# Kernel optimization log

Hardware: AMD Instinct MI355X
Metric: run time of the kernel (lower is better)

The kernel has to match this reference:

```python
import jax, jax.numpy as jnp
import numpy as np

N, E, D, L = 50000, 800000, 128, 2
EPS = 1e-7

def _logmap0(y):
    # Poincare ball (c=1) logmap at origin: artanh(||y||) * y / ||y||
    n = jnp.linalg.norm(y, axis=-1, keepdims=True)
    nc = jnp.clip(n, EPS, 1.0 - 1e-5)
    return jnp.arctanh(nc) * y / jnp.maximum(n, EPS)

def _expmap0(u):
    # Poincare ball (c=1) expmap at origin: tanh(||u||) * u / ||u||
    n = jnp.linalg.norm(u, axis=-1, keepdims=True)
    return jnp.tanh(n) * u / jnp.maximum(n, EPS)

def _l2norm(x):
    # F.normalize(p=2, dim=1)
    return x / jnp.maximum(jnp.linalg.norm(x, axis=1, keepdims=True), 1e-12)

def setup_inputs() -> dict:
    key = jax.random.key(0)
    ks = jax.random.split(key, 12)
    src = jax.random.randint(ks[0], (E,), 0, N)
    dst = jax.random.randint(ks[1], (E,), 0, N)
    e_emb = jax.random.normal(ks[2], (N, D), jnp.float32)
    b_emb = jax.random.normal(ks[3], (N, D), jnp.float32) * 0.1  # inside Poincare ball
    s_emb = jax.random.normal(ks[4], (N, D), jnp.float32)
    sc = 0.05
    eW = jax.random.normal(ks[5], (L, D, D), jnp.float32) * sc
    eB = jax.random.normal(ks[6], (L, D), jnp.float32) * sc
    bW = jax.random.normal(ks[7], (L, D, D), jnp.float32) * sc
    bB = jax.random.normal(ks[8], (L, D), jnp.float32) * sc
    sW = jax.random.normal(ks[9], (L, D, D), jnp.float32) * sc
    sB = jax.random.normal(ks[10], (L, D), jnp.float32) * sc
    return dict(e_emb=e_emb, b_emb=b_emb, s_emb=s_emb, eW=eW, eB=eB,
                bW=bW, bB=bB, sW=sW, sB=sB, src=src, dst=dst)

def reference(e_emb, b_emb, s_emb, eW, eB, bW, bB, sW, sB, src, dst):
    n_nodes = e_emb.shape[0]
    ones_e = jnp.ones(src.shape[0], jnp.float32)
    in_deg = jax.ops.segment_sum(ones_e, dst, num_segments=n_nodes)
    out_deg = jax.ops.segment_sum(ones_e, src, num_segments=n_nodes)
    # DGL GraphConv norm='both': D_out^{-1/2} (sum over in-neighbors) D_in^{-1/2}
    norm_out = jnp.where(out_deg > 0, out_deg ** -0.5, 0.0)[:, None]
    norm_in = jnp.where(in_deg > 0, in_deg ** -0.5, 0.0)[:, None]
    inv_in = jnp.where(in_deg > 0, 1.0 / in_deg, 0.0)[:, None]  # mean reduce

    def agg_sum(h):
        return jax.ops.segment_sum(h[src], dst, num_segments=n_nodes)

    for l in range(L):
        # Euclidean branch: GraphConv(norm='both') then LeakyReLU(0.2)
        h = agg_sum(e_emb * norm_out) * norm_in
        e_emb = jax.nn.leaky_relu(h @ eW[l].T + eB[l], negative_slope=0.2)
        # Hyperbolic branch: logmap0 -> Linear -> neighbor mean -> expmap0
        tan_b = _logmap0(b_emb) @ bW[l].T + bB[l]
        b_emb = _expmap0(agg_sum(tan_b) * inv_in)
        # Spherical branch: normalize -> Linear -> neighbor mean -> normalize
        tan_s = _l2norm(s_emb) @ sW[l].T + sB[l]
        s_emb = _l2norm(agg_sum(tan_s) * inv_in)
    return (e_emb, b_emb, s_emb)
```

## Files before the change

### kernel.cpp

```cpp
#include <hip/hip_runtime.h>
#include <math.h>

#define DD 128
#define PSTRIDE 384

typedef _Float16 half8 __attribute__((ext_vector_type(8)));
typedef float floatx4 __attribute__((ext_vector_type(4)));

__device__ __forceinline__ float g16_sum(float x) {
#pragma unroll
  for (int m = 8; m >= 1; m >>= 1) x += __shfl_xor(x, m, 64);
  return x;
}
__device__ __forceinline__ int wave_sum_i(int x) {
#pragma unroll
  for (int m = 32; m >= 1; m >>= 1) x += __shfl_xor(x, m, 64);
  return x;
}

__global__ void deg_wcvt_kernel(const int* __restrict__ src, const int* __restrict__ dst,
                                int* __restrict__ out_deg8, int* __restrict__ in_deg8,
                                int* __restrict__ rank8, int E, int N,
                                const float* __restrict__ eW, const float* __restrict__ bW,
                                const float* __restrict__ sW, _Float16* __restrict__ Wh, int nW,
                                int DB) {
  int bx = blockIdx.x;
  if (bx < DB) {
    int e = bx * 256 + threadIdx.x;
    if (e < E) {
      int h = e & 7;
      atomicAdd(&out_deg8[h * N + src[e]], 1);
      rank8[e] = atomicAdd(&in_deg8[h * N + dst[e]], 1);
    }
  } else {
    int i = (bx - DB) * 256 + threadIdx.x;
    if (i < nW) {
      Wh[i]          = (_Float16)eW[i];
      Wh[i + nW]     = (_Float16)bW[i];
      Wh[i + 2 * nW] = (_Float16)sW[i];
    }
  }
}

__global__ void norms_psum_kernel(const int* __restrict__ in_deg8, const int* __restrict__ out_deg8,
                                  int* __restrict__ in_deg, float* __restrict__ norm_in,
                                  float* __restrict__ norm_out, float* __restrict__ inv_in,
                                  int* __restrict__ part, int N) {
  __shared__ int wsum[4];
  int t = threadIdx.x, lane = t & 63, w = t >> 6;
  int i = blockIdx.x * 256 + t;
  int di = 0;
  if (i < N) {
    int dq = 0;
#pragma unroll
    for (int h = 0; h < 8; ++h) {
      di += in_deg8[h * N + i];
      dq += out_deg8[h * N + i];
    }
    in_deg[i] = di;
    norm_in[i]  = di > 0 ? 1.0f / sqrtf((float)di) : 0.0f;
    norm_out[i] = dq > 0 ? 1.0f / sqrtf((float)dq) : 0.0f;
    inv_in[i]   = di > 0 ? 1.0f / (float)di : 0.0f;
  }
  int s = wave_sum_i(di);
  if (lane == 0) wsum[w] = s;
  __syncthreads();
  if (t == 0) part[blockIdx.x] = wsum[0] + wsum[1] + wsum[2] + wsum[3];
}

__global__ void part_scan_kernel(int* __restrict__ part, int nb) {
  __shared__ int wsum[4];
  int t = threadIdx.x, lane = t & 63, w = t >> 6;
  int x = (t < nb) ? part[t] : 0;
  int v = x;
#pragma unroll
  for (int off = 1; off < 64; off <<= 1) {
    int y = __shfl_up(v, off, 64);
    if (lane >= off) v += y;
  }
  if (lane == 63) wsum[w] = v;
  __syncthreads();
  int base = 0;
  for (int j = 0; j < w; ++j) base += wsum[j];
  if (t < nb) part[t] = base + v - x;
}

__global__ void local_scan_kernel(const int* __restrict__ deg, const int* __restrict__ part,
                                  int* __restrict__ row_off, int* __restrict__ in_deg8,
                                  int N, int E) {
  __shared__ int wsum[4];
  int t = threadIdx.x, lane = t & 63, w = t >> 6;
  int i = blockIdx.x * 256 + t;
  int x = (i < N) ? deg[i] : 0;
  int v = x;
#pragma unroll
  for (int off = 1; off < 64; off <<= 1) {
    int y = __shfl_up(v, off, 64);
    if (lane >= off) v += y;
  }
  if (lane == 63) wsum[w] = v;
  __syncthreads();
  int base = 0;
  for (int j = 0; j < w; ++j) base += wsum[j];
  if (i < N) {
    int ro = part[blockIdx.x] + base + v - x;
    row_off[i] = ro;
    int cum = ro;
#pragma unroll
    for (int h = 0; h < 8; ++h) {
      int c = in_deg8[h * N + i];
      in_deg8[h * N + i] = cum;
      cum += c;
    }
  }
  if (blockIdx.x == 0 && t == 0) row_off[N] = E;
}

__device__ __forceinline__ void gemm0_tile(int part, int rb, const float* __restrict__ A,
                                           const _Float16* __restrict__ Wh,
                                           const float* __restrict__ Bb,
                                           _Float16* __restrict__ Q, int N) {
  int t = threadIdx.x, lane = t & 63, w = t >> 6;
  int m = lane & 15, quad = lane >> 4, c0 = w * 32;
  int rbase = rb * 64;
  _Float16* Qo = Q + part * DD;
  half8 bf[2][4];
#pragma unroll
  for (int tj = 0; tj < 2; ++tj)
#pragma unroll
    for (int kk = 0; kk < 4; ++kk)
      bf[tj][kk] = *(const half8*)&Wh[(c0 + tj * 16 + m) * DD + kk * 32 + quad * 8];
  float bias0 = 0.f, bias1 = 0.f;
  if (part) { bias0 = Bb[c0 + m]; bias1 = Bb[c0 + 16 + m]; }
#pragma unroll
  for (int r = 0; r < 4; ++r) {
    int row0 = r * 16;
    int arow = rbase + row0 + m; if (arow >= N) arow = N - 1;
    const float* Ap = A + (size_t)arow * DD;
    half8 af[4];
    float nsq = 0.f;
#pragma unroll
    for (int kk = 0; kk < 4; ++kk) {
      float4 x0 = *(const float4*)&Ap[kk * 32 + quad * 8];
      float4 x1 = *(const float4*)&Ap[kk * 32 + quad * 8 + 4];
      if (part)
        nsq += x0.x * x0.x + x0.y * x0.y + x0.z * x0.z + x0.w * x0.w +
               x1.x * x1.x + x1.y * x1.y + x1.z * x1.z + x1.w * x1.w;
      half8 a;
      a[0] = (_Float16)x0.x; a[1] = (_Float16)x0.y; a[2] = (_Float16)x0.z; a[3] = (_Float16)x0.w;
      a[4] = (_Float16)x1.x; a[5] = (_Float16)x1.y; a[6] = (_Float16)x1.z; a[7] = (_Float16)x1.w;
      af[kk] = a;
    }
    float fr = 1.f;
    if (part) {
      nsq += __shfl_xor(nsq, 16, 64);
      nsq += __shfl_xor(nsq, 32, 64);
      float n = sqrtf(nsq);
      if (part == 1) {
        float nc = fminf(fmaxf(n, 1e-7f), 1.0f - 1e-5f);
        fr = atanhf(nc) / fmaxf(n, 1e-7f);
      } else {
        fr = 1.0f / fmaxf(n, 1e-12f);
      }
    }
    floatx4 acc0 = {0.f, 0.f, 0.f, 0.f}, acc1 = {0.f, 0.f, 0.f, 0.f};
#pragma unroll
    for (int kk = 0; kk < 4; ++kk) {
      acc0 = __builtin_amdgcn_mfma_f32_16x16x32_f16(af[kk], bf[0][kk], acc0, 0, 0, 0);
      acc1 = __builtin_amdgcn_mfma_f32_16x16x32_f16(af[kk], bf[1][kk], acc1, 0, 0, 0);
    }
    int vrow = rbase + row0 + quad * 4;
#pragma unroll
    for (int reg = 0; reg < 4; ++reg) {
      int v = vrow + reg;
      float fs = part ? __shfl(fr, quad * 4 + reg, 64) : 1.f;
      if (v < N) {
        Qo[(size_t)v * PSTRIDE + c0 + m]      = (_Float16)(acc0[reg] * fs + bias0);
        Qo[(size_t)v * PSTRIDE + c0 + 16 + m] = (_Float16)(acc1[reg] * fs + bias1);
      }
    }
  }
}

__device__ __forceinline__ void gemm_tile(int part, int rb, const _Float16* __restrict__ P,
                                          const _Float16* __restrict__ Wh,
                                          const float* __restrict__ Bb,
                                          _Float16* __restrict__ Q, int N) {
  int t = threadIdx.x, lane = t & 63, w = t >> 6;
  int m = lane & 15, quad = lane >> 4, c0 = w * 32;
  int rbase = rb * 64;
  const _Float16* Ain = P + part * DD;
  _Float16* Qo = Q + part * DD;
  half8 bf[2][4];
#pragma unroll
  for (int tj = 0; tj < 2; ++tj)
#pragma unroll
    for (int kk = 0; kk < 4; ++kk)
      bf[tj][kk] = *(const half8*)&Wh[(c0 + tj * 16 + m) * DD + kk * 32 + quad * 8];
  float bias0 = 0.f, bias1 = 0.f;
  if (Bb) { bias0 = Bb[c0 + m]; bias1 = Bb[c0 + 16 + m]; }
#pragma unroll
  for (int r = 0; r < 4; ++r) {
    int row0 = r * 16;
    int arow = rbase + row0 + m; if (arow >= N) arow = N - 1;
    const _Float16* Ap = Ain + (size_t)arow * PSTRIDE;
    floatx4 acc0 = {0.f, 0.f, 0.f, 0.f}, acc1 = {0.f, 0.f, 0.f, 0.f};
#pragma unroll
    for (int kk = 0; kk < 4; ++kk) {
      half8 af = *(const half8*)&Ap[kk * 32 + quad * 8];
      acc0 = __builtin_amdgcn_mfma_f32_16x16x32_f16(af, bf[0][kk], acc0, 0, 0, 0);
      acc1 = __builtin_amdgcn_mfma_f32_16x16x32_f16(af, bf[1][kk], acc1, 0, 0, 0);
    }
    int vrow = rbase + row0 + quad * 4;
#pragma unroll
    for (int reg = 0; reg < 4; ++reg) {
      int v = vrow + reg;
      if (v < N) {
        Qo[(size_t)v * PSTRIDE + c0 + m]      = (_Float16)(acc0[reg] + bias0);
        Qo[(size_t)v * PSTRIDE + c0 + 16 + m] = (_Float16)(acc1[reg] + bias1);
      }
    }
  }
}

__global__ __launch_bounds__(256) void fill_gemm0_kernel(
    const int* __restrict__ src, const int* __restrict__ dst,
    const int* __restrict__ rank8, const int* __restrict__ bin_base,
    const float* __restrict__ norm_out, int2* __restrict__ csr_sw, int E,
    const float* __restrict__ e0, const float* __restrict__ b0, const float* __restrict__ s0,
    const _Float16* __restrict__ WhE, const _Float16* __restrict__ WhB,
    const _Float16* __restrict__ WhS, const float* __restrict__ bBl,
    const float* __restrict__ sBl, _Float16* __restrict__ Q, int N, int FB, int GB) {
  int bx = blockIdx.x;
  if (bx < FB) {
    int e = bx * 256 + threadIdx.x;
    if (e < E) {
      int d = dst[e], s = src[e];
      int h = e & 7;
      int pos = bin_base[h * N + d] + rank8[e];
      csr_sw[pos] = make_int2(s, __float_as_int(norm_out[s]));
    }
  } else {
    int gb = bx - FB;
    int part = gb / GB, rb = gb % GB;
    const float* A = (part == 0) ? e0 : (part == 1 ? b0 : s0);
    const _Float16* Wh = (part == 0) ? WhE : (part == 1 ? WhB : WhS);
    const float* Bb = (part == 0) ? nullptr : (part == 1 ? bBl : sBl);
    gemm0_tile(part, rb, A, Wh, Bb, Q, N);
  }
}

__global__ __launch_bounds__(256) void gemm3_kernel(const _Float16* __restrict__ P,
                                                    const _Float16* __restrict__ WhE,
                                                    const _Float16* __restrict__ WhB,
                                                    const _Float16* __restrict__ WhS,
                                                    const float* __restrict__ bBl,
                                                    const float* __restrict__ sBl,
                                                    _Float16* __restrict__ Q, int N) {
  int part = blockIdx.y;
  const _Float16* Wh = (part == 0) ? WhE : (part == 1 ? WhB : WhS);
  const float* Bb = (part == 0) ? nullptr : (part == 1 ? bBl : sBl);
  gemm_tile(part, blockIdx.x, P, Wh, Bb, Q, N);
}

__global__ __launch_bounds__(256) void agg_fused_kernel(
    const _Float16* __restrict__ Q, const int* __restrict__ row_off,
    const int2* __restrict__ csr_sw, const float* __restrict__ norm_in,
    const float* __restrict__ inv_in, const float* __restrict__ eBias,
    float* __restrict__ oe, float* __restrict__ ob, float* __restrict__ os,
    _Float16* __restrict__ Pnext, int N, int write_pack, int write_out) {
  int lane = threadIdx.x & 63;
  int v = blockIdx.x * 4 + (threadIdx.x >> 6);
  if (v >= N) return;
  int g = lane >> 4, q = lane & 15;
  int beg = row_off[v], end = row_off[v + 1];
  float eacc[8], bacc[8], sacc[8];
#pragma unroll
  for (int j = 0; j < 8; ++j) { eacc[j] = 0.f; bacc[j] = 0.f; sacc[j] = 0.f; }
  int i = beg;
  for (; i + 8 <= end; i += 8) {
    int2 swa = csr_sw[i + g];
    int2 swb = csr_sw[i + 4 + g];
    float wa = __int_as_float(swa.y), wb = __int_as_float(swb.y);
    const _Float16* ra = Q + (size_t)swa.x * PSTRIDE + q * 8;
    const _Float16* rb = Q + (size_t)swb.x * PSTRIDE + q * 8;
    half8 ea = *(const half8*)ra;
    half8 e2 = *(const half8*)rb;
    half8 ba = *(const half8*)(ra + 128);
    half8 b2 = *(const half8*)(rb + 128);
    half8 sa = *(const half8*)(ra + 256);
    half8 s2 = *(const half8*)(rb + 256);
#pragma unroll
    for (int j = 0; j < 8; ++j) {
      eacc[j] += wa * (float)ea[j];
      eacc[j] += wb * (float)e2[j];
      bacc[j] += (float)ba[j];
      bacc[j] += (float)b2[j];
      sacc[j] += (float)sa[j];
      sacc[j] += (float)s2[j];
    }
  }
  if (i + 4 <= end) {
    int2 sw = csr_sw[i + g];
    float wgt = __int_as_float(sw.y);
    const _Float16* rp = Q + (size_t)sw.x * PSTRIDE + q * 8;
    half8 ev = *(const half8*)rp;
    half8 bv = *(const half8*)(rp + 128);
    half8 sv = *(const half8*)(rp + 256);
#pragma unroll
    for (int j = 0; j < 8; ++j) {
      eacc[j] += wgt * (float)ev[j];
      bacc[j] += (float)bv[j];
      sacc[j] += (float)sv[j];
    }
    i += 4;
  }
  if (i + g < end) {
    int2 sw = csr_sw[i + g];
    float wgt = __int_as_float(sw.y);
    const _Float16* rp = Q + (size_t)sw.x * PSTRIDE + q * 8;
    half8 ev = *(const half8*)rp;
    half8 bv = *(const half8*)(rp + 128);
    half8 sv = *(const half8*)(rp + 256);
#pragma unroll
    for (int j = 0; j < 8; ++j) {
      eacc[j] += wgt * (float)ev[j];
      bacc[j] += (float)bv[j];
      sacc[j] += (float)sv[j];
    }
  }
#pragma unroll
  for (int j = 0; j < 8; ++j) {
    eacc[j] += __shfl_xor(eacc[j], 16, 64);
    eacc[j] += __shfl_xor(eacc[j], 32, 64);
    bacc[j] += __shfl_xor(bacc[j], 16, 64);
    bacc[j] += __shfl_xor(bacc[j], 32, 64);
    sacc[j] += __shfl_xor(sacc[j], 16, 64);
    sacc[j] += __shfl_xor(sacc[j], 32, 64);
  }
  float ni = norm_in[v], iv = inv_in[v];
  const float4* ebp = (const float4*)eBias;
  float4 eb0 = ebp[q * 2], eb1 = ebp[q * 2 + 1];
  float bias[8] = {eb0.x, eb0.y, eb0.z, eb0.w, eb1.x, eb1.y, eb1.z, eb1.w};
  float h[8], ub[8], us[8];
  float ss2 = 0.f;
#pragma unroll
  for (int j = 0; j < 8; ++j) {
    float t = eacc[j] * ni + bias[j];
    h[j] = t > 0.f ? t : 0.2f * t;
    ub[j] = bacc[j] * iv;
    us[j] = sacc[j] * iv; ss2 += us[j] * us[j];
  }
  float ns = sqrtf(g16_sum(ss2));
  float fs = 1.0f / fmaxf(ns, 1e-12f);
  if (write_out) {
    float bs2 = 0.f;
#pragma unroll
    for (int j = 0; j < 8; ++j) bs2 += ub[j] * ub[j];
    float nb = sqrtf(g16_sum(bs2));
    float fb = tanhf(nb) / fmaxf(nb, 1e-7f);
    if (g == 0) {
      float4* p = (float4*)(oe + (size_t)v * DD);
      p[q * 2]     = make_float4(h[0], h[1], h[2], h[3]);
      p[q * 2 + 1] = make_float4(h[4], h[5], h[6], h[7]);
    } else if (g == 1) {
      float4* p = (float4*)(ob + (size_t)v * DD);
      p[q * 2]     = make_float4(ub[0] * fb, ub[1] * fb, ub[2] * fb, ub[3] * fb);
      p[q * 2 + 1] = make_float4(ub[4] * fb, ub[5] * fb, ub[6] * fb, ub[7] * fb);
    } else if (g == 2) {
      float4* p = (float4*)(os + (size_t)v * DD);
      p[q * 2]     = make_float4(us[0] * fs, us[1] * fs, us[2] * fs, us[3] * fs);
      p[q * 2 + 1] = make_float4(us[4] * fs, us[5] * fs, us[6] * fs, us[7] * fs);
    }
  }
  if (write_pack) {
    if (g == 3) {
      half8 he, hb, hs;
#pragma unroll
      for (int j = 0; j < 8; ++j) {
        he[j] = (_Float16)h[j];
        hb[j] = (_Float16)ub[j];
        hs[j] = (_Float16)(us[j] * fs);
      }
      _Float16* Pr = Pnext + (size_t)v * PSTRIDE + q * 8;
      *(half8*)&Pr[0]   = he;
      *(half8*)&Pr[128] = hb;
      *(half8*)&Pr[256] = hs;
    }
  }
}

extern "C" void kernel_launch(void* const* d_in, const int* in_sizes, int n_in,
                              void* d_out, int out_size, void* d_ws, size_t ws_size,
                              hipStream_t stream) {
  const float* e0 = (const float*)d_in[0];
  const float* b0 = (const float*)d_in[1];
  const float* s0 = (const float*)d_in[2];
  const float* eW = (const float*)d_in[3];
  const float* eB = (const float*)d_in[4];
  const float* bW = (const float*)d_in[5];
  const float* bB = (const float*)d_in[6];
  const float* sW = (const float*)d_in[7];
  const float* sB = (const float*)d_in[8];
  const int* src = (const int*)d_in[9];
  const int* dst = (const int*)d_in[10];
  int N = in_sizes[0] / DD;
  int E = in_sizes[9];
  int L = in_sizes[3] / (DD * DD);
  int LDD2 = L * DD * DD;

  char* w = (char*)d_ws;
  int* in_deg8  = (int*)w; w += (size_t)8 * N * 4;
  int* out_deg8 = (int*)w; w += (size_t)8 * N * 4;
  int* rank8    = (int*)w; w += (size_t)E * 4;
  int* in_deg   = (int*)w; w += (size_t)N * 4;
  int* row_off  = (int*)w; w += (size_t)(N + 4) * 4;
  int* pscan    = (int*)w; w += (size_t)1024 * 4;
  int2* csr_sw  = (int2*)w; w += (size_t)E * 8;
  float* norm_in  = (float*)w; w += (size_t)N * 4;
  float* norm_out = (float*)w; w += (size_t)N * 4;
  float* inv_in   = (float*)w; w += (size_t)N * 4;
  w = (char*)(((size_t)w + 255) & ~(size_t)255);
  _Float16* P = (_Float16*)w; w += (size_t)N * PSTRIDE * 2;
  _Float16* Q = (_Float16*)w; w += (size_t)N * PSTRIDE * 2;
  _Float16* Wh = (_Float16*)w; w += (size_t)3 * LDD2 * 2;
  _Float16* whE = Wh;
  _Float16* whB = Wh + LDD2;
  _Float16* whS = Wh + 2 * LDD2;

  float* oe = (float*)d_out;
  float* ob = oe + (size_t)N * DD;
  float* os = ob + (size_t)N * DD;

  int DB = (E + 255) / 256;
  int AB = (N + 3) / 4;
  int GB = (N + 63) / 64;
  int WB = (LDD2 + 255) / 256;
  int PB = (N + 255) / 256;

  hipMemsetAsync(d_ws, 0, (size_t)16 * N * 4, stream);
  deg_wcvt_kernel<<<DB + WB, 256, 0, stream>>>(src, dst, out_deg8, in_deg8, rank8, E, N,
                                               eW, bW, sW, Wh, LDD2, DB);
  norms_psum_kernel<<<PB, 256, 0, stream>>>(in_deg8, out_deg8, in_deg,
                                            norm_in, norm_out, inv_in, pscan, N);
  part_scan_kernel<<<1, 256, 0, stream>>>(pscan, PB);
  local_scan_kernel<<<PB, 256, 0, stream>>>(in_deg, pscan, row_off, in_deg8, N, E);
  fill_gemm0_kernel<<<DB + 3 * GB, 256, 0, stream>>>(src, dst, rank8, in_deg8, norm_out,
                                                     csr_sw, E, e0, b0, s0,
                                                     whE, whB, whS, bB, sB, Q, N, DB, GB);
  agg_fused_kernel<<<AB, 256, 0, stream>>>(Q, row_off, csr_sw, norm_in, inv_in, eB,
                                           oe, ob, os, P, N,
                                           (L > 1) ? 1 : 0, (L == 1) ? 1 : 0);
  for (int l = 1; l < L; ++l) {
    size_t lo = (size_t)l * DD * DD;
    gemm3_kernel<<<dim3(GB, 3), 256, 0, stream>>>(P, whE + lo, whB + lo, whS + lo,
                                                  bB + (size_t)l * DD, sB + (size_t)l * DD, Q, N);
    agg_fused_kernel<<<AB, 256, 0, stream>>>(Q, row_off, csr_sw, norm_in, inv_in,
                                             eB + (size_t)l * DD, oe, ob, os, P, N,
                                             (l < L - 1) ? 1 : 0, (l == L - 1) ? 1 : 0);
  }
}
```

Before: 482.2 us.

## Fold source norm into GEMM output, shrink CSR to indices, overlap hyperbolic/spherical GEMM with degree pass

```diff
diff --git a/kernel.cpp b/kernel.cpp
--- a/kernel.cpp
+++ b/kernel.cpp
@@ -18,107 +18,9 @@
   return x;
 }
 
-__global__ void deg_wcvt_kernel(const int* __restrict__ src, const int* __restrict__ dst,
-                                int* __restrict__ out_deg8, int* __restrict__ in_deg8,
-                                int* __restrict__ rank8, int E, int N,
-                                const float* __restrict__ eW, const float* __restrict__ bW,
-                                const float* __restrict__ sW, _Float16* __restrict__ Wh, int nW,
-                                int DB) {
-  int bx = blockIdx.x;
-  if (bx < DB) {
-    int e = bx * 256 + threadIdx.x;
-    if (e < E) {
-      int h = e & 7;
-      atomicAdd(&out_deg8[h * N + src[e]], 1);
-      rank8[e] = atomicAdd(&in_deg8[h * N + dst[e]], 1);
-    }
-  } else {
-    int i = (bx - DB) * 256 + threadIdx.x;
-    if (i < nW) {
-      Wh[i]          = (_Float16)eW[i];
-      Wh[i + nW]     = (_Float16)bW[i];
-      Wh[i + 2 * nW] = (_Float16)sW[i];
-    }
-  }
-}
-
-__global__ void norms_psum_kernel(const int* __restrict__ in_deg8, const int* __restrict__ out_deg8,
-                                  int* __restrict__ in_deg, float* __restrict__ norm_in,
-                                  float* __restrict__ norm_out, float* __restrict__ inv_in,
-                                  int* __restrict__ part, int N) {
-  __shared__ int wsum[4];
-  int t = threadIdx.x, lane = t & 63, w = t >> 6;
-  int i = blockIdx.x * 256 + t;
-  int di = 0;
-  if (i < N) {
-    int dq = 0;
-#pragma unroll
-    for (int h = 0; h < 8; ++h) {
-      di += in_deg8[h * N + i];
-      dq += out_deg8[h * N + i];
-    }
-    in_deg[i] = di;
-    norm_in[i]  = di > 0 ? 1.0f / sqrtf((float)di) : 0.0f;
-    norm_out[i] = dq > 0 ? 1.0f / sqrtf((float)dq) : 0.0f;
-    inv_in[i]   = di > 0 ? 1.0f / (float)di : 0.0f;
-  }
-  int s = wave_sum_i(di);
-  if (lane == 0) wsum[w] = s;
-  __syncthreads();
-  if (t == 0) part[blockIdx.x] = wsum[0] + wsum[1] + wsum[2] + wsum[3];
-}
-
-__global__ void part_scan_kernel(int* __restrict__ part, int nb) {
-  __shared__ int wsum[4];
-  int t = threadIdx.x, lane = t & 63, w = t >> 6;
-  int x = (t < nb) ? part[t] : 0;
-  int v = x;
-#pragma unroll
-  for (int off = 1; off < 64; off <<= 1) {
-    int y = __shfl_up(v, off, 64);
-    if (lane >= off) v += y;
-  }
-  if (lane == 63) wsum[w] = v;
-  __syncthreads();
-  int base = 0;
-  for (int j = 0; j < w; ++j) base += wsum[j];
-  if (t < nb) part[t] = base + v - x;
-}
-
-__global__ void local_scan_kernel(const int* __restrict__ deg, const int* __restrict__ part,
-                                  int* __restrict__ row_off, int* __restrict__ in_deg8,
-                                  int N, int E) {
-  __shared__ int wsum[4];
-  int t = threadIdx.x, lane = t & 63, w = t >> 6;
-  int i = blockIdx.x * 256 + t;
-  int x = (i < N) ? deg[i] : 0;
-  int v = x;
-#pragma unroll
-  for (int off = 1; off < 64; off <<= 1) {
-    int y = __shfl_up(v, off, 64);
-    if (lane >= off) v += y;
-  }
-  if (lane == 63) wsum[w] = v;
-  __syncthreads();
-  int base = 0;
-  for (int j = 0; j < w; ++j) base += wsum[j];
-  if (i < N) {
-    int ro = part[blockIdx.x] + base + v - x;
-    row_off[i] = ro;
-    int cum = ro;
-#pragma unroll
-    for (int h = 0; h < 8; ++h) {
-      int c = in_deg8[h * N + i];
-      in_deg8[h * N + i] = cum;
-      cum += c;
-    }
-  }
-  if (blockIdx.x == 0 && t == 0) row_off[N] = E;
-}
-
 __device__ __forceinline__ void gemm0_tile(int part, int rb, const float* __restrict__ A,
-                                           const _Float16* __restrict__ Wh,
-                                           const float* __restrict__ Bb,
+                                           const float* __restrict__ Wf, const float* __restrict__ Bb,
+                                           const float* __restrict__ norm_out,
                                            _Float16* __restrict__ Q, int N) {
   int t = threadIdx.x, lane = t & 63, w = t >> 6;
   int m = lane & 15, quad = lane >> 4, c0 = w * 32;
@@ -128,8 +30,15 @@
 #pragma unroll
   for (int tj = 0; tj < 2; ++tj)
 #pragma unroll
-    for (int kk = 0; kk < 4; ++kk)
-      bf[tj][kk] = *(const half8*)&Wh[(c0 + tj * 16 + m) * DD + kk * 32 + quad * 8];
+    for (int kk = 0; kk < 4; ++kk) {
+      const float* wp = &Wf[(c0 + tj * 16 + m) * DD + kk * 32 + quad * 8];
+      float4 w0 = *(const float4*)wp;
+      float4 w1 = *(const float4*)(wp + 4);
+      half8 hv;
+      hv[0] = (_Float16)w0.x; hv[1] = (_Float16)w0.y; hv[2] = (_Float16)w0.z; hv[3] = (_Float16)w0.w;
+      hv[4] = (_Float16)w1.x; hv[5] = (_Float16)w1.y; hv[6] = (_Float16)w1.z; hv[7] = (_Float16)w1.w;
+      bf[tj][kk] = hv;
+    }
   float bias0 = 0.f, bias1 = 0.f;
   if (part) { bias0 = Bb[c0 + m]; bias1 = Bb[c0 + 16 + m]; }
 #pragma unroll
@@ -173,18 +82,19 @@
 #pragma unroll
     for (int reg = 0; reg < 4; ++reg) {
       int v = vrow + reg;
-      float fs = part ? __shfl(fr, quad * 4 + reg, 64) : 1.f;
+      float fshfl = __shfl(fr, quad * 4 + reg, 64);
       if (v < N) {
-        Qo[(size_t)v * PSTRIDE + c0 + m]      = (_Float16)(acc0[reg] * fs + bias0);
-        Qo[(size_t)v * PSTRIDE + c0 + 16 + m] = (_Float16)(acc1[reg] * fs + bias1);
+        float sc = part ? fshfl : norm_out[v];
+        Qo[(size_t)v * PSTRIDE + c0 + m]      = (_Float16)(acc0[reg] * sc + bias0);
+        Qo[(size_t)v * PSTRIDE + c0 + 16 + m] = (_Float16)(acc1[reg] * sc + bias1);
       }
     }
   }
 }
 
 __device__ __forceinline__ void gemm_tile(int part, int rb, const _Float16* __restrict__ P,
-                                          const _Float16* __restrict__ Wh,
-                                          const float* __restrict__ Bb,
+                                          const float* __restrict__ Wf, const float* __restrict__ Bb,
+                                          const float* __restrict__ norm_out,
                                           _Float16* __restrict__ Q, int N) {
   int t = threadIdx.x, lane = t & 63, w = t >> 6;
   int m = lane & 15, quad = lane >> 4, c0 = w * 32;
@@ -195,10 +105,17 @@
 #pragma unroll
   for (int tj = 0; tj < 2; ++tj)
 #pragma unroll
-    for (int kk = 0; kk < 4; ++kk)
-      bf[tj][kk] = *(const half8*)&Wh[(c0 + tj * 16 + m) * DD + kk * 32 + quad * 8];
+    for (int kk = 0; kk < 4; ++kk) {
+      const float* wp = &Wf[(c0 + tj * 16 + m) * DD + kk * 32 + quad * 8];
+      float4 w0 = *(const float4*)wp;
+      float4 w1 = *(const float4*)(wp + 4);
+      half8 hv;
+      hv[0] = (_Float16)w0.x; hv[1] = (_Float16)w0.y; hv[2] = (_Float16)w0.z; hv[3] = (_Float16)w0.w;
+      hv[4] = (_Float16)w1.x; hv[5] = (_Float16)w1.y; hv[6] = (_Float16)w1.z; hv[7] = (_Float16)w1.w;
+      bf[tj][kk] = hv;
+    }
   float bias0 = 0.f, bias1 = 0.f;
-  if (Bb) { bias0 = Bb[c0 + m]; bias1 = Bb[c0 + 16 + m]; }
+  if (part) { bias0 = Bb[c0 + m]; bias1 = Bb[c0 + 16 + m]; }
 #pragma unroll
   for (int r = 0; r < 4; ++r) {
     int row0 = r * 16;
@@ -216,56 +133,170 @@
     for (int reg = 0; reg < 4; ++reg) {
       int v = vrow + reg;
       if (v < N) {
-        Qo[(size_t)v * PSTRIDE + c0 + m]      = (_Float16)(acc0[reg] + bias0);
-        Qo[(size_t)v * PSTRIDE + c0 + 16 + m] = (_Float16)(acc1[reg] + bias1);
+        float sc = part ? 1.f : norm_out[v];
+        Qo[(size_t)v * PSTRIDE + c0 + m]      = (_Float16)(acc0[reg] * sc + bias0);
+        Qo[(size_t)v * PSTRIDE + c0 + 16 + m] = (_Float16)(acc1[reg] * sc + bias1);
       }
     }
   }
 }
 
-__global__ __launch_bounds__(256) void fill_gemm0_kernel(
+__global__ __launch_bounds__(256) void deg_gemmbs_kernel(
+    const int* __restrict__ src, const int* __restrict__ dst,
+    int* __restrict__ out8, int* __restrict__ in8, int* __restrict__ rank8, int E, int N,
+    const float* __restrict__ b0, const float* __restrict__ s0,
+    const float* __restrict__ bW, const float* __restrict__ sW,
+    const float* __restrict__ bB, const float* __restrict__ sB,
+    float* __restrict__ norm_out_unused, _Float16* __restrict__ Q, int DB, int GBt) {
+  int bx = blockIdx.x;
+  if (bx < DB) {
+    int g = bx * 256 + (int)threadIdx.x;
+    int e0i = g * 4;
+    if (e0i + 3 < E) {
+      int4 s4 = ((const int4*)src)[g];
+      int4 d4 = ((const int4*)dst)[g];
+      atomicAdd(&out8[((e0i    ) & 7) * N + s4.x], 1);
+      atomicAdd(&out8[((e0i + 1) & 7) * N + s4.y], 1);
+      atomicAdd(&out8[((e0i + 2) & 7) * N + s4.z], 1);
+      atomicAdd(&out8[((e0i + 3) & 7) * N + s4.w], 1);
+      int4 r;
+      r.x = atomicAdd(&in8[((e0i    ) & 7) * N + d4.x], 1);
+      r.y = atomicAdd(&in8[((e0i + 1) & 7) * N + d4.y], 1);
+      r.z = atomicAdd(&in8[((e0i + 2) & 7) * N + d4.z], 1);
+      r.w = atomicAdd(&in8[((e0i + 3) & 7) * N + d4.w], 1);
+      ((int4*)rank8)[g] = r;
+    } else if (e0i < E) {
+      for (int e = e0i; e < E; ++e) {
+        atomicAdd(&out8[(e & 7) * N + src[e]], 1);
+        rank8[e] = atomicAdd(&in8[(e & 7) * N + dst[e]], 1);
+      }
+    }
+  } else {
+    int gt = bx - DB;
+    int part = 1 + gt / GBt, rb = gt % GBt;
+    const float* A  = (part == 1) ? b0 : s0;
+    const float* Wf = (part == 1) ? bW : sW;
+    const float* Bb = (part == 1) ? bB : sB;
+    gemm0_tile(part, rb, A, Wf, Bb, norm_out_unused, Q, N);
+  }
+}
+
+__global__ void norms_psum_kernel(const int* __restrict__ in8, const int* __restrict__ out8,
+                                  int* __restrict__ in_deg, float* __restrict__ norm_in,
+                                  float* __restrict__ norm_out, float* __restrict__ inv_in,
+                                  int* __restrict__ part, int N) {
+  __shared__ int wsum[4];
+  int t = threadIdx.x, lane = t & 63, w = t >> 6;
+  int i = blockIdx.x * 256 + t;
+  int di = 0;
+  if (i < N) {
+    int dq = 0;
+#pragma unroll
+    for (int h = 0; h < 8; ++h) { di += in8[h * N + i]; dq += out8[h * N + i]; }
+    in_deg[i] = di;
+    norm_in[i]  = di > 0 ? 1.0f / sqrtf((float)di) : 0.0f;
+    norm_out[i] = dq > 0 ? 1.0f / sqrtf((float)dq) : 0.0f;
+    inv_in[i]   = di > 0 ? 1.0f / (float)di : 0.0f;
+  }
+  int s = wave_sum_i(di);
+  if (lane == 0) wsum[w] = s;
+  __syncthreads();
+  if (t == 0) part[blockIdx.x] = wsum[0] + wsum[1] + wsum[2] + wsum[3];
+}
+
+__global__ void part_scan_kernel(int* __restrict__ part, int nb) {
+  __shared__ int wsum[4];
+  int t = threadIdx.x, lane = t & 63, w = t >> 6;
+  int x = (t < nb) ? part[t] : 0;
+  int v = x;
+#pragma unroll
+  for (int off = 1; off < 64; off <<= 1) {
+    int y = __shfl_up(v, off, 64);
+    if (lane >= off) v += y;
+  }
+  if (lane == 63) wsum[w] = v;
+  __syncthreads();
+  int base = 0;
+  for (int j = 0; j < w; ++j) base += wsum[j];
+  if (t < nb) part[t] = base + v - x;
+}
+
+__global__ void local_scan_kernel(const int* __restrict__ deg, const int* __restrict__ part,
+                                  int* __restrict__ row_off, int* __restrict__ in8,
+                                  int N, int E) {
+  __shared__ int wsum[4];
+  int t = threadIdx.x, lane = t & 63, w = t >> 6;
+  int i = blockIdx.x * 256 + t;
+  int x = (i < N) ? deg[i] : 0;
+  int v = x;
+#pragma unroll
+  for (int off = 1; off < 64; off <<= 1) {
+    int y = __shfl_up(v, off, 64);
+    if (lane >= off) v += y;
+  }
+  if (lane == 63) wsum[w] = v;
+  __syncthreads();
+  int base = 0;
+  for (int j = 0; j < w; ++j) base += wsum[j];
+  if (i < N) {
+    int ro = part[blockIdx.x] + base + v - x;
+    row_off[i] = ro;
+    int cum = ro;
+#pragma unroll
+    for (int h = 0; h < 8; ++h) {
+      int cb = in8[h * N + i];
+      in8[h * N + i] = cum;
+      cum += cb;
+    }
+  }
+  if (blockIdx.x == 0 && t == 0) row_off[N] = E;
+}
+
+__global__ __launch_bounds__(256) void fill_gemme_kernel(
     const int* __restrict__ src, const int* __restrict__ dst,
     const int* __restrict__ rank8, const int* __restrict__ bin_base,
-    const float* __restrict__ norm_out, int2* __restrict__ csr_sw, int E,
-    const float* __restrict__ e0, const float* __restrict__ b0, const float* __restrict__ s0,
-    const _Float16* __restrict__ WhE, const _Float16* __restrict__ WhB,
-    const _Float16* __restrict__ WhS, const float* __restrict__ bBl,
-    const float* __restrict__ sBl, _Float16* __restrict__ Q, int N, int FB, int GB) {
+    int* __restrict__ csr, int E,
+    const float* __restrict__ e0, const float* __restrict__ eW,
+    const float* __restrict__ norm_out, _Float16* __restrict__ Q, int N, int FB, int GBt) {
   int bx = blockIdx.x;
   if (bx < FB) {
-    int e = bx * 256 + threadIdx.x;
-    if (e < E) {
-      int d = dst[e], s = src[e];
-      int h = e & 7;
-      int pos = bin_base[h * N + d] + rank8[e];
-      csr_sw[pos] = make_int2(s, __float_as_int(norm_out[s]));
+    int g = bx * 256 + (int)threadIdx.x;
+    int e0i = g * 4;
+    if (e0i + 3 < E) {
+      int4 s4 = ((const int4*)src)[g];
+      int4 d4 = ((const int4*)dst)[g];
+      int4 r4 = ((const int4*)rank8)[g];
+      csr[bin_base[((e0i    ) & 7) * N + d4.x] + r4.x] = s4.x;
+      csr[bin_base[((e0i + 1) & 7) * N + d4.y] + r4.y] = s4.y;
+      csr[bin_base[((e0i + 2) & 7) * N + d4.z] + r4.z] = s4.z;
+      csr[bin_base[((e0i + 3) & 7) * N + d4.w] + r4.w] = s4.w;
+    } else if (e0i < E) {
+      for (int e = e0i; e < E; ++e)
+        csr[bin_base[(e & 7) * N + dst[e]] + rank8[e]] = src[e];
     }
   } else {
-    int gb = bx - FB;
-    int part = gb / GB, rb = gb % GB;
-    const float* A = (part == 0) ? e0 : (part == 1 ? b0 : s0);
-    const _Float16* Wh = (part == 0) ? WhE : (part == 1 ? WhB : WhS);
-    const float* Bb = (part == 0) ? nullptr : (part == 1 ? bBl : sBl);
-    gemm0_tile(part, rb, A, Wh, Bb, Q, N);
+    gemm0_tile(0, bx - FB, e0, eW, nullptr, norm_out, Q, N);
   }
 }
 
 __global__ __launch_bounds__(256) void gemm3_kernel(const _Float16* __restrict__ P,
-                                                    const _Float16* __restrict__ WhE,
-                                                    const _Float16* __restrict__ WhB,
-                                                    const _Float16* __restrict__ WhS,
+                                                    const float* __restrict__ eWl,
+                                                    const float* __restrict__ bWl,
+                                                    const float* __restrict__ sWl,
                                                     const float* __restrict__ bBl,
                                                     const float* __restrict__ sBl,
-                                                    _Float16* __restrict__ Q, int N) {
-  int part = blockIdx.y;
-  const _Float16* Wh = (part == 0) ? WhE : (part == 1 ? WhB : WhS);
-  const float* Bb = (part == 0) ? nullptr : (part == 1 ? bBl : sBl);
-  gemm_tile(part, blockIdx.x, P, Wh, Bb, Q, N);
+                                                    const float* __restrict__ norm_out,
+                                                    _Float16* __restrict__ Q, int N, int GBt) {
+  int gt = blockIdx.x;
+  int part = gt / GBt, rb = gt % GBt;
+  const float* Wf = (part == 0) ? eWl : (part == 1 ? bWl : sWl);
+  const float* Bb = (part == 1) ? bBl : sBl;
+  gemm_tile(part, rb, P, Wf, Bb, norm_out, Q, N);
 }
 
 __global__ __launch_bounds__(256) void agg_fused_kernel(
     const _Float16* __restrict__ Q, const int* __restrict__ row_off,
-    const int2* __restrict__ csr_sw, const float* __restrict__ norm_in,
+    const int* __restrict__ csr, const float* __restrict__ norm_in,
     const float* __restrict__ inv_in, const float* __restrict__ eBias,
     float* __restrict__ oe, float* __restrict__ ob, float* __restrict__ os,
     _Float16* __restrict__ Pnext, int N, int write_pack, int write_out) {
@@ -279,11 +310,9 @@
   for (int j = 0; j < 8; ++j) { eacc[j] = 0.f; bacc[j] = 0.f; sacc[j] = 0.f; }
   int i = beg;
   for (; i + 8 <= end; i += 8) {
-    int2 swa = csr_sw[i + g];
-    int2 swb = csr_sw[i + 4 + g];
-    float wa = __int_as_float(swa.y), wb = __int_as_float(swb.y);
-    const _Float16* ra = Q + (size_t)swa.x * PSTRIDE + q * 8;
-    const _Float16* rb = Q + (size_t)swb.x * PSTRIDE + q * 8;
+    int na = csr[i + g], nb2 = csr[i + 4 + g];
+    const _Float16* ra = Q + (size_t)na * PSTRIDE + q * 8;
+    const _Float16* rb = Q + (size_t)nb2 * PSTRIDE + q * 8;
     half8 ea = *(const half8*)ra;
     half8 e2 = *(const half8*)rb;
     half8 ba = *(const half8*)(ra + 128);
@@ -292,39 +321,34 @@
     half8 s2 = *(const half8*)(rb + 256);
 #pragma unroll
     for (int j = 0; j < 8; ++j) {
-      eacc[j] += wa * (float)ea[j];
-      eacc[j] += wb * (float)e2[j];
-      bacc[j] += (float)ba[j];
-      bacc[j] += (float)b2[j];
-      sacc[j] += (float)sa[j];
-      sacc[j] += (float)s2[j];
+      eacc[j] += (float)ea[j]; eacc[j] += (float)e2[j];
+      bacc[j] += (float)ba[j]; bacc[j] += (float)b2[j];
+      sacc[j] += (float)sa[j]; sacc[j] += (float)s2[j];
     }
   }
   if (i + 4 <= end) {
-    int2 sw = csr_sw[i + g];
-    float wgt = __int_as_float(sw.y);
-    const _Float16* rp = Q + (size_t)sw.x * PSTRIDE + q * 8;
+    int na = csr[i + g];
+    const _Float16* rp = Q + (size_t)na * PSTRIDE + q * 8;
     half8 ev = *(const half8*)rp;
     half8 bv = *(const half8*)(rp + 128);
     half8 sv = *(const half8*)(rp + 256);
 #pragma unroll
     for (int j = 0; j < 8; ++j) {
-      eacc[j] += wgt * (float)ev[j];
+      eacc[j] += (float)ev[j];
       bacc[j] += (float)bv[j];
       sacc[j] += (float)sv[j];
     }
     i += 4;
   }
   if (i + g < end) {
-    int2 sw = csr_sw[i + g];
-    float wgt = __int_as_float(sw.y);
-    const _Float16* rp = Q + (size_t)sw.x * PSTRIDE + q * 8;
+    int na = csr[i + g];
+    const _Float16* rp = Q + (size_t)na * PSTRIDE + q * 8;
     half8 ev = *(const half8*)rp;
     half8 bv = *(const half8*)(rp + 128);
     half8 sv = *(const half8*)(rp + 256);
 #pragma unroll
     for (int j = 0; j < 8; ++j) {
-      eacc[j] += wgt * (float)ev[j];
+      eacc[j] += (float)ev[j];
       bacc[j] += (float)bv[j];
       sacc[j] += (float)sv[j];
     }
@@ -346,8 +370,8 @@
   float ss2 = 0.f;
 #pragma unroll
   for (int j = 0; j < 8; ++j) {
-    float t = eacc[j] * ni + bias[j];
-    h[j] = t > 0.f ? t : 0.2f * t;
+    float tt = eacc[j] * ni + bias[j];
+    h[j] = tt > 0.f ? tt : 0.2f * tt;
     ub[j] = bacc[j] * iv;
     us[j] = sacc[j] * iv; ss2 += us[j] * us[j];
   }
@@ -373,20 +397,18 @@
       p[q * 2 + 1] = make_float4(us[4] * fs, us[5] * fs, us[6] * fs, us[7] * fs);
     }
   }
-  if (write_pack) {
-    if (g == 3) {
-      half8 he, hb, hs;
-#pragma unroll
-      for (int j = 0; j < 8; ++j) {
-        he[j] = (_Float16)h[j];
-        hb[j] = (_Float16)ub[j];
-        hs[j] = (_Float16)(us[j] * fs);
-      }
-      _Float16* Pr = Pnext + (size_t)v * PSTRIDE + q * 8;
-      *(half8*)&Pr[0]   = he;
-      *(half8*)&Pr[128] = hb;
-      *(half8*)&Pr[256] = hs;
-    }
+  if (write_pack && g == 3) {
+    half8 he, hb, hs;
+#pragma unroll
+    for (int j = 0; j < 8; ++j) {
+      he[j] = (_Float16)h[j];
+      hb[j] = (_Float16)ub[j];
+      hs[j] = (_Float16)(us[j] * fs);
+    }
+    _Float16* Pr = Pnext + (size_t)v * PSTRIDE + q * 8;
+    *(half8*)&Pr[0]   = he;
+    *(half8*)&Pr[128] = hb;
+    *(half8*)&Pr[256] = hs;
   }
 }
 
@@ -407,7 +429,6 @@
   int N = in_sizes[0] / DD;
   int E = in_sizes[9];
   int L = in_sizes[3] / (DD * DD);
-  int LDD2 = L * DD * DD;
 
   char* w = (char*)d_ws;
   int* in_deg8  = (int*)w; w += (size_t)8 * N * 4;
@@ -416,47 +437,42 @@
   int* in_deg   = (int*)w; w += (size_t)N * 4;
   int* row_off  = (int*)w; w += (size_t)(N + 4) * 4;
   int* pscan    = (int*)w; w += (size_t)1024 * 4;
-  int2* csr_sw  = (int2*)w; w += (size_t)E * 8;
+  int* csr      = (int*)w; w += (size_t)E * 4;
   float* norm_in  = (float*)w; w += (size_t)N * 4;
   float* norm_out = (float*)w; w += (size_t)N * 4;
   float* inv_in   = (float*)w; w += (size_t)N * 4;
   w = (char*)(((size_t)w + 255) & ~(size_t)255);
   _Float16* P = (_Float16*)w; w += (size_t)N * PSTRIDE * 2;
   _Float16* Q = (_Float16*)w; w += (size_t)N * PSTRIDE * 2;
-  _Float16* Wh = (_Float16*)w; w += (size_t)3 * LDD2 * 2;
-  _Float16* whE = Wh;
-  _Float16* whB = Wh + LDD2;
-  _Float16* whS = Wh + 2 * LDD2;
 
   float* oe = (float*)d_out;
   float* ob = oe + (size_t)N * DD;
   float* os = ob + (size_t)N * DD;
 
-  int DB = (E + 255) / 256;
-  int AB = (N + 3) / 4;
-  int GB = (N + 63) / 64;
-  int WB = (LDD2 + 255) / 256;
-  int PB = (N + 255) / 256;
+  int DB  = (E + 1023) / 1024;
+  int ABt = (N + 3) / 4;
+  int GBt = (N + 63) / 64;
+  int NC  = (N + 255) / 256;
 
   hipMemsetAsync(d_ws, 0, (size_t)16 * N * 4, stream);
-  deg_wcvt_kernel<<<DB + WB, 256, 0, stream>>>(src, dst, out_deg8, in_deg8, rank8, E, N,
-                                               eW, bW, sW, Wh, LDD2, DB);
-  norms_psum_kernel<<<PB, 256, 0, stream>>>(in_deg8, out_deg8, in_deg,
+  deg_gemmbs_kernel<<<DB + 2 * GBt, 256, 0, stream>>>(src, dst, out_deg8, in_deg8, rank8, E, N,
+                                                      b0, s0, bW, sW, bB, sB, norm_out, Q, DB, GBt);
+  norms_psum_kernel<<<NC, 256, 0, stream>>>(in_deg8, out_deg8, in_deg,
                                             norm_in, norm_out, inv_in, pscan, N);
-  part_scan_kernel<<<1, 256, 0, stream>>>(pscan, PB);
-  local_scan_kernel<<<PB, 256, 0, stream>>>(in_deg, pscan, row_off, in_deg8, N, E);
-  fill_gemm0_kernel<<<DB + 3 * GB, 256, 0, stream>>>(src, dst, rank8, in_deg8, norm_out,
-                                                     csr_sw, E, e0, b0, s0,
-                                                     whE, whB, whS, bB, sB, Q, N, DB, GB);
-  agg_fused_kernel<<<AB, 256, 0, stream>>>(Q, row_off, csr_sw, norm_in, inv_in, eB,
-                                           oe, ob, os, P, N,
-                                           (L > 1) ? 1 : 0, (L == 1) ? 1 : 0);
+  part_scan_kernel<<<1, 256, 0, stream>>>(pscan, NC);
+  local_scan_kernel<<<NC, 256, 0, stream>>>(in_deg, pscan, row_off, in_deg8, N, E);
+  fill_gemme_kernel<<<DB + GBt, 256, 0, stream>>>(src, dst, rank8, in_deg8, csr, E,
+                                                  e0, eW, norm_out, Q, N, DB, GBt);
+  agg_fused_kernel<<<ABt, 256, 0, stream>>>(Q, row_off, csr, norm_in, inv_in, eB,
+                                            oe, ob, os, P, N,
+                                            (L > 1) ? 1 : 0, (L == 1) ? 1 : 0);
   for (int l = 1; l < L; ++l) {
     size_t lo = (size_t)l * DD * DD;
-    gemm3_kernel<<<dim3(GB, 3), 256, 0, stream>>>(P, whE + lo, whB + lo, whS + lo,
-                                                  bB + (size_t)l * DD, sB + (size_t)l * DD, Q, N);
-    agg_fused_kernel<<<AB, 256, 0, stream>>>(Q, row_off, csr_sw, norm_in, inv_in,
-                                             eB + (size_t)l * DD, oe, ob, os, P, N,
-                                             (l < L - 1) ? 1 : 0, (l == L - 1) ? 1 : 0);
-  }
-}
+    gemm3_kernel<<<3 * GBt, 256, 0, stream>>>(P, eW + lo, bW + lo, sW + lo,
+                                              bB + (size_t)l * DD, sB + (size_t)l * DD,
+                                              norm_out, Q, N, GBt);
+    agg_fused_kernel<<<ABt, 256, 0, stream>>>(Q, row_off, csr, norm_in, inv_in,
+                                              eB + (size_t)l * DD, oe, ob, os, P, N,
+                                              (l < L - 1) ? 1 : 0, (l == L - 1) ? 1 : 0);
+  }
+}
```

New measurement: 522.1 us. 1.08x slower.
